# Kernel tuning notes

Measured on AMD Instinct MI355X. Metric: run time of the kernel, lower is better.

Reference implementation:

```python
import jax, jax.numpy as jnp
import numpy as np
from jax import lax

K, D = 7, 2                      # kernel_size, dilation
PAD = (K - 1) * D                # = 12, matches init padding
B, CIN, COUT, L = 8, 128, 256, 4096


def _na_indices(L2, k, d):
    """NATTEN-style dilated 1D neighborhood: key positions + rel-pos-bias indices."""
    i = jnp.arange(L2)
    r, ii = i % d, i // d
    Lg = (L2 - r + d - 1) // d                       # dilation-group lengths
    start = jnp.clip(ii - k // 2, 0, Lg - k)         # clamped window start (in-group)
    t = jnp.arange(k)
    pos = r[:, None] + d * (start[:, None] + t[None, :])        # [L2,k] key positions
    bidx = start[:, None] + t[None, :] - ii[:, None] + (k - 1)  # [L2,k] rpb index in [0,2k-2]
    return pos, bidx


def setup_inputs() -> dict:
    key = jax.random.key(0)
    ks = jax.random.split(key, 11)
    s = 0.05
    return {
        "x": jax.random.normal(ks[0], (B, CIN, L), jnp.float32),
        "conv1_v": jax.random.normal(ks[1], (COUT, CIN, K), jnp.float32) * s,
        "conv1_g": jax.random.uniform(ks[2], (COUT,), jnp.float32, 0.5, 1.5),
        "conv1_b": jax.random.normal(ks[3], (COUT,), jnp.float32) * s,
        "qkv_w": jax.random.normal(ks[4], (3 * COUT, COUT), jnp.float32) * s,
        "qkv_b": jax.random.normal(ks[5], (3 * COUT,), jnp.float32) * s,
        "rpb": jax.random.normal(ks[6], (1, 2 * K - 1), jnp.float32) * s,
        "proj_w": jax.random.normal(ks[7], (COUT, COUT), jnp.float32) * s,
        "proj_b": jax.random.normal(ks[8], (COUT,), jnp.float32) * s,
        "ds_w": jax.random.normal(ks[9], (COUT, CIN, 1), jnp.float32) * s,
        "ds_b": jax.random.normal(ks[10], (COUT,), jnp.float32) * s,
    }


def reference(x, conv1_v, conv1_g, conv1_b, qkv_w, qkv_b, rpb, proj_w, proj_b, ds_w, ds_b):
    # weight_norm: w = g * v / ||v|| over (in_ch, kernel) per out channel
    vn = jnp.sqrt(jnp.sum(conv1_v * conv1_v, axis=(1, 2), keepdims=True))
    w1 = conv1_g[:, None, None] * conv1_v / vn
    out = lax.conv_general_dilated(x, w1, (1,), [(PAD, PAD)], rhs_dilation=(D,),
                                   dimension_numbers=("NCH", "OIH", "NCH"))
    out = out + conv1_b[None, :, None]
    out = jax.nn.relu(out[:, :, :-PAD])              # chomp1 + relu (dropout = eval identity)

    # left-pad then neighborhood attention on [B, L2, C]
    h = jnp.pad(out, ((0, 0), (0, 0), (PAD, 0))).transpose(0, 2, 1)
    L2 = h.shape[1]
    qkv = h @ qkv_w.T + qkv_b
    q, k_, v = jnp.split(qkv, 3, axis=-1)            # single head, head_dim = COUT
    pos, bidx = _na_indices(L2, K, D)
    kg = k_[:, pos, :]                               # [B, L2, K, C]
    vg = v[:, pos, :]
    scores = jnp.einsum("blc,blkc->blk", q * (COUT ** -0.5), kg) + rpb[0][bidx][None]
    attn = jax.nn.softmax(scores, axis=-1)
    o = jnp.einsum("blk,blkc->blc", attn, vg) @ proj_w.T + proj_b

    out = jax.nn.relu(o.transpose(0, 2, 1)[:, :, :-PAD])   # chomp2 + relu
    res = jnp.einsum("bcl,oc->bol", x, ds_w[:, :, 0]) + ds_b[None, :, None]
    return jax.nn.relu(out + res)
```

## Files before the change

kernel.cpp:

```cpp
#include <hip/hip_runtime.h>
#include <math.h>

#define KW 7
#define PADW 12
#define BATCH 8
#define CIN 128
#define COUT 256
#define LEN 4096
#define L2V 4108
#define NQKV 768
#define KCONV 896
#define PTILE 128

typedef unsigned short u16;
typedef short v8s __attribute__((ext_vector_type(8)));
typedef float v4f __attribute__((ext_vector_type(4)));

#define KEY3(r) ((((r) & 3) ^ (((r) >> 2) & 1)))

__device__ __forceinline__ u16 f2bf(float f) {
  unsigned int x = __float_as_uint(f);
  x += 0x7fffu + ((x >> 16) & 1u);
  return (u16)(x >> 16);
}
__device__ __forceinline__ float bf2f(u16 u) {
  return __uint_as_float(((unsigned int)u) << 16);
}

__device__ __forceinline__ void gll16(const void* g, void* l) {
  __builtin_amdgcn_global_load_lds(
      (const __attribute__((address_space(1))) void*)g,
      (__attribute__((address_space(3))) void*)l, 16, 0, 0);
}

__device__ __forceinline__ void wait_vm(int n) {
  switch (n) {
    case 0:  asm volatile("s_waitcnt vmcnt(0)" ::: "memory"); break;
    case 2:  asm volatile("s_waitcnt vmcnt(2)" ::: "memory"); break;
    case 3:  asm volatile("s_waitcnt vmcnt(3)" ::: "memory"); break;
    case 10: asm volatile("s_waitcnt vmcnt(10)" ::: "memory"); break;
  }
}
#define LGKM0()  asm volatile("s_waitcnt lgkmcnt(0)" ::: "memory")
#define BARRIER() { __builtin_amdgcn_s_barrier(); asm volatile("" ::: "memory"); }

#define MFMA16(ACC, AA, BB)                                                    \
  { _Pragma("unroll") for (int fi_ = 0; fi_ < 4; ++fi_)                        \
    _Pragma("unroll") for (int fj_ = 0; fj_ < 4; ++fj_)                        \
      ACC[fi_][fj_] = __builtin_amdgcn_mfma_f32_16x16x32_bf16(                 \
          AA[fi_], BB[fj_], ACC[fi_][fj_], 0, 0, 0); }

__global__ __launch_bounds__(256) void prep_wn(
    const float* __restrict__ v, const float* __restrict__ g,
    u16* __restrict__ wt)
{
  const int c = blockIdx.x;
  const float* vo = v + (size_t)c * (CIN * KW);
  float s = 0.f;
  for (int i = threadIdx.x; i < CIN * KW; i += 256) { float t = vo[i]; s += t * t; }
#pragma unroll
  for (int off = 1; off < 64; off <<= 1) s += __shfl_xor(s, off);
  __shared__ float red[4];
  if ((threadIdx.x & 63) == 0) red[threadIdx.x >> 6] = s;
  __syncthreads();
  const float tot = red[0] + red[1] + red[2] + red[3];
  const float scale = g[c] / sqrtf(tot);
  for (int i = threadIdx.x; i < CIN * KW; i += 256) {
    const int ci = i / 7, t = i - ci * 7;
    wt[((size_t)c * KW + t) * CIN + ci] = f2bf(vo[i] * scale);
  }
}

__global__ __launch_bounds__(256) void prep_cast(
    const float* __restrict__ qw, const float* __restrict__ pw,
    const float* __restrict__ dw, u16* __restrict__ qwb,
    u16* __restrict__ pwb, u16* __restrict__ dwb)
{
  const int i4 = (blockIdx.x * 256 + threadIdx.x) * 4;
  const float* src; u16* dst; int off;
  if (i4 < 196608)      { src = qw; dst = qwb; off = i4; }
  else if (i4 < 262144) { src = pw; dst = pwb; off = i4 - 196608; }
  else                  { src = dw; dst = dwb; off = i4 - 262144; }
  const float4 vv = *(const float4*)(src + off);
  *(ushort4*)(dst + off) = make_ushort4(f2bf(vv.x), f2bf(vv.y), f2bf(vv.z), f2bf(vv.w));
}

__global__ __launch_bounds__(256) void zero_fill(
    u16* __restrict__ xT, u16* __restrict__ qkv, const float* __restrict__ qb)
{
  const int idx = blockIdx.x * 256 + threadIdx.x;
  if (idx < BATCH * PADW * CIN) {
    const int b = idx / (PADW * CIN), r = idx - b * (PADW * CIN);
    xT[(size_t)b * L2V * CIN + r] = 0;
  } else {
    const int k = idx - BATCH * PADW * CIN;
    const int b = k / (PADW * NQKV), r2 = k - b * (PADW * NQKV);
    const int row = r2 / NQKV, n = r2 - row * NQKV;
    qkv[((size_t)b * L2V + row) * NQKV + n] = f2bf(qb[n]);
  }
}

__global__ __launch_bounds__(256) void xpose(const float* __restrict__ x, u16* __restrict__ xT)
{
  const int b = blockIdx.y, p0 = blockIdx.x * 64;
  const int tx = threadIdx.x & 15, ty = threadIdx.x >> 4;
  const int p = p0 + ty * 4;
  const float* xb = x + (size_t)b * CIN * LEN;
  u16* xTb = xT + (size_t)b * L2V * CIN + (size_t)(PADW + p) * CIN;
#pragma unroll
  for (int half = 0; half < 2; ++half) {
    const int ci0 = half * 64 + tx * 4;
    float r[4][4];
#pragma unroll
    for (int i = 0; i < 4; ++i)
      *(float4*)r[i] = *(const float4*)(xb + (size_t)(ci0 + i) * LEN + p);
#pragma unroll
    for (int j = 0; j < 4; ++j)
      *(ushort4*)(xTb + (size_t)j * CIN + ci0) =
          make_ushort4(f2bf(r[0][j]), f2bf(r[1][j]), f2bf(r[2][j]), f2bf(r[3][j]));
  }
}

__global__ __launch_bounds__(512, 2) void conv_qkv_fused(
    const u16* __restrict__ wt, const u16* __restrict__ xT,
    const float* __restrict__ c1b, const u16* __restrict__ qwb,
    const float* __restrict__ qb, u16* __restrict__ qkv)
{
  const int b = blockIdx.y;
  const int p0 = blockIdx.x * PTILE;
  const int tid = threadIdx.x;
  const int w = tid >> 6, lane = tid & 63;
  const int l15 = lane & 15, kg = lane >> 4;
  const int wA = w >> 1, wB = w & 1;

  __shared__ u16 hA[PTILE * 256];
  __shared__ u16 pool[40960];

  const u16* xTb = xT + (size_t)b * L2V * CIN + (size_t)p0 * CIN;

  v4f acc[4][4];
#pragma unroll
  for (int i = 0; i < 4; ++i)
#pragma unroll
    for (int j = 0; j < 4; ++j) acc[i][j] = (v4f){0.f, 0.f, 0.f, 0.f};

  auto stageA = [&](int s, int buf) {
    const int t = s >> 2, ci0 = (s & 3) << 5;
    u16* dst = pool + buf * 12288;
#pragma unroll
    for (int i = 0; i < 2; ++i) {
      const int cidx = i * 512 + tid;
      const int row = cidx >> 2, ch = cidx & 3;
      gll16(wt + (size_t)row * KCONV + t * CIN + ci0 + ((ch ^ KEY3(row)) << 3),
            (void*)(dst + cidx * 8));
    }
    {
      const int row = tid >> 2, ch = tid & 3;
      gll16(xTb + (size_t)(2 * t + row) * CIN + ci0 + ((ch ^ KEY3(row)) << 3),
            (void*)(dst + 8192 + tid * 8));
    }
  };

  stageA(0, 0);
  stageA(1, 1);

#pragma unroll
  for (int s = 0; s < 28; ++s) {
    if (s < 27) wait_vm(3); else wait_vm(0);
    BARRIER()
    if (s < 26) stageA(s + 2, (s + 2) % 3);
    const u16* wbuf = pool + (s % 3) * 12288;
    const u16* xbuf = wbuf + 8192;
    v8s a[4], bb[4];
#pragma unroll
    for (int f = 0; f < 4; ++f) {
      const int c = wA * 64 + f * 16 + l15;
      a[f] = *(const v8s*)&wbuf[c * 32 + ((kg ^ KEY3(c)) << 3)];
      const int p = wB * 64 + f * 16 + l15;
      bb[f] = *(const v8s*)&xbuf[p * 32 + ((kg ^ KEY3(p)) << 3)];
    }
    MFMA16(acc, a, bb)
  }

#pragma unroll
  for (int fi = 0; fi < 4; ++fi) {
    const int cb = wA * 64 + fi * 16 + kg * 4;
    const float4 bv = *(const float4*)(c1b + cb);
    const int ch32 = cb >> 3, off = cb & 7;
#pragma unroll
    for (int fj = 0; fj < 4; ++fj) {
      const int p = wB * 64 + fj * 16 + l15;
      *(ushort4*)&hA[p * 256 + ((ch32 ^ (p & 7)) << 3) + off] = make_ushort4(
          f2bf(fmaxf(acc[fi][fj][0] + bv.x, 0.f)),
          f2bf(fmaxf(acc[fi][fj][1] + bv.y, 0.f)),
          f2bf(fmaxf(acc[fi][fj][2] + bv.z, 0.f)),
          f2bf(fmaxf(acc[fi][fj][3] + bv.w, 0.f)));
      acc[fi][fj] = (v4f){0.f, 0.f, 0.f, 0.f};
    }
  }
  LGKM0();
  BARRIER()

  auto stageB = [&](int it2, int buf) {
    const int nt = it2 >> 3, k0 = (it2 & 7) << 5;
    u16* dst = pool + buf * 8192;
#pragma unroll
    for (int i = 0; i < 2; ++i) {
      const int cidx = i * 512 + tid;
      const int row = cidx >> 2, ch = cidx & 3;
      gll16(qwb + (size_t)(nt * 256 + row) * COUT + k0 + ((ch ^ KEY3(row)) << 3),
            (void*)(dst + cidx * 8));
    }
  };
  stageB(0, 0);
  stageB(1, 1);

  const size_t mg0 = (size_t)b * L2V + PADW + p0;
  u16* T = pool + 24576;

#pragma unroll
  for (int it = 0; it < 24; ++it) {
    const int s = it & 7, st = it >> 3;
    if (it == 23) wait_vm(0);
    else if (it >= 8 && s <= 1) wait_vm(10);
    else wait_vm(2);
    BARRIER()
    if (it < 22) stageB(it + 2, (it + 2) % 3);
    const u16* nbuf = pool + (it % 3) * 8192;
    v8s a[4], bb[4];
#pragma unroll
    for (int f = 0; f < 4; ++f) {
      const int n = wA * 64 + f * 16 + l15;
      a[f] = *(const v8s*)&nbuf[n * 32 + ((kg ^ KEY3(n)) << 3)];
      const int m = wB * 64 + f * 16 + l15;
      bb[f] = *(const v8s*)&hA[m * 256 + ((((s << 2) + kg) ^ (m & 7)) << 3)];
    }
    MFMA16(acc, a, bb)

    if (s == 7) {
#pragma unroll
      for (int h2 = 0; h2 < 2; ++h2) {
        if ((wA >> 1) == h2) {
#pragma unroll
          for (int fi = 0; fi < 4; ++fi) {
            const int j = (wA & 1) * 64 + fi * 16 + kg * 4;
            const float4 bv = *(const float4*)(qb + st * 256 + h2 * 128 + j);
            const int jc = j >> 3, joff = j & 7;
#pragma unroll
            for (int fj = 0; fj < 4; ++fj) {
              const int m = wB * 64 + fj * 16 + l15;
              *(ushort4*)&T[m * 128 + ((jc ^ (m & 15)) << 3) + joff] = make_ushort4(
                  f2bf(acc[fi][fj][0] + bv.x), f2bf(acc[fi][fj][1] + bv.y),
                  f2bf(acc[fi][fj][2] + bv.z), f2bf(acc[fi][fj][3] + bv.w));
            }
          }
        }
        LGKM0();
        BARRIER()
#pragma unroll
        for (int i2 = 0; i2 < 4; ++i2) {
          const int chunk = i2 * 512 + tid;
          const int m = chunk >> 4, j16 = chunk & 15;
          const int4 vv = *(const int4*)&T[m * 128 + ((j16 ^ (m & 15)) << 3)];
          *(int4*)(qkv + (mg0 + m) * NQKV + st * 256 + h2 * 128 + j16 * 8) = vv;
        }
        LGKM0();
        BARRIER()
      }
#pragma unroll
      for (int fi = 0; fi < 4; ++fi)
#pragma unroll
        for (int fj = 0; fj < 4; ++fj) acc[fi][fj] = (v4f){0.f, 0.f, 0.f, 0.f};
    }
  }
}

__global__ __launch_bounds__(256) void attn_bf16(
    const u16* __restrict__ qkv, const float* __restrict__ rpb,
    u16* __restrict__ ao)
{
  const int wid = (blockIdx.x << 2) + (threadIdx.x >> 6);
  const int lane = threadIdx.x & 63;
  const int b = wid >> 12;
  const int j = wid & 4095;
  const int r = j & 1, ii = j >> 1;
  int start = ii - 3;
  start = start < 0 ? 0 : start;
  start = start > 2047 ? 2047 : start;

  const u16* base = qkv + (size_t)b * L2V * NQKV;
  const ushort4 qv = *(const ushort4*)(base + (size_t)j * NQKV + 4 * lane);
  const float q0 = bf2f(qv.x) * 0.0625f, q1 = bf2f(qv.y) * 0.0625f;
  const float q2 = bf2f(qv.z) * 0.0625f, q3 = bf2f(qv.w) * 0.0625f;

  float sc[7];
  float mx = -1e30f;
#pragma unroll
  for (int t = 0; t < 7; ++t) {
    const int pos = r + 2 * (start + t);
    const ushort4 kv = *(const ushort4*)(base + (size_t)pos * NQKV + COUT + 4 * lane);
    float s = q0 * bf2f(kv.x) + q1 * bf2f(kv.y) + q2 * bf2f(kv.z) + q3 * bf2f(kv.w);
#pragma unroll
    for (int o = 1; o < 64; o <<= 1) s += __shfl_xor(s, o);
    s += rpb[start + t - ii + 6];
    sc[t] = s;
    mx = fmaxf(mx, s);
  }
  float sum = 0.f;
#pragma unroll
  for (int t = 0; t < 7; ++t) { sc[t] = __expf(sc[t] - mx); sum += sc[t]; }
  const float inv = 1.f / sum;

  float a0 = 0.f, a1 = 0.f, a2 = 0.f, a3 = 0.f;
#pragma unroll
  for (int t = 0; t < 7; ++t) {
    const int pos = r + 2 * (start + t);
    const ushort4 vv = *(const ushort4*)(base + (size_t)pos * NQKV + 2 * COUT + 4 * lane);
    const float wgt = sc[t] * inv;
    a0 += wgt * bf2f(vv.x); a1 += wgt * bf2f(vv.y);
    a2 += wgt * bf2f(vv.z); a3 += wgt * bf2f(vv.w);
  }
  *(ushort4*)(ao + ((size_t)(b * LEN + j)) * COUT + 4 * lane) =
      make_ushort4(f2bf(a0), f2bf(a1), f2bf(a2), f2bf(a3));
}

__global__ __launch_bounds__(256, 2) void projds_gll(
    const u16* __restrict__ ao, const u16* __restrict__ pwb,
    const float* __restrict__ pb, const u16* __restrict__ xT,
    const u16* __restrict__ dwb, const float* __restrict__ db,
    float* __restrict__ out)
{
  const int b = blockIdx.z;
  const int l0 = blockIdx.x * 128, o0 = blockIdx.y * 128;
  const int tid = threadIdx.x;
  const int w = tid >> 6, lane = tid & 63;
  const int l15 = lane & 15, kg = lane >> 4;
  const int wr = w >> 1, wc = w & 1;

  __shared__ u16 sX[2][128 * 32];
  __shared__ u16 sW[2][128 * 32];

  const int arow = tid >> 2, ach = tid & 3;
  const int akey = KEY3(arow);
  const u16* aob = ao + (size_t)b * LEN * COUT;
  const u16* xTb = xT + ((size_t)b * L2V + PADW) * CIN;

  auto stage1 = [&](int s, int buf) {
#pragma unroll
    for (int i = 0; i < 2; ++i) {
      const int row = i * 64 + arow;
      const int sl = (ach ^ akey) << 3;
      gll16(aob + (size_t)(l0 + row) * COUT + (s << 5) + sl,
            (void*)&sX[buf][(i * 256 + tid) * 8]);
      gll16(pwb + (size_t)(o0 + row) * COUT + (s << 5) + sl,
            (void*)&sW[buf][(i * 256 + tid) * 8]);
    }
  };
  auto stage2 = [&](int s, int buf) {
#pragma unroll
    for (int i = 0; i < 2; ++i) {
      const int row = i * 64 + arow;
      const int sl = (ach ^ akey) << 3;
      gll16(xTb + (size_t)(l0 + row) * CIN + (s << 5) + sl,
            (void*)&sX[buf][(i * 256 + tid) * 8]);
      gll16(dwb + (size_t)(o0 + row) * CIN + (s << 5) + sl,
            (void*)&sW[buf][(i * 256 + tid) * 8]);
    }
  };

  v4f acc[4][4];
#pragma unroll
  for (int i = 0; i < 4; ++i)
#pragma unroll
    for (int j = 0; j < 4; ++j) acc[i][j] = (v4f){0.f, 0.f, 0.f, 0.f};

  stage1(0, 0);
  __syncthreads();
  for (int ss = 0; ss < 12; ++ss) {
    const int buf = ss & 1;
    if (ss < 7) stage1(ss + 1, buf ^ 1);
    else if (ss < 11) stage2(ss - 7, buf ^ 1);
    v8s a[4], bb[4];
#pragma unroll
    for (int f = 0; f < 4; ++f) {
      const int lr = wr * 64 + f * 16 + l15;
      a[f] = *(const v8s*)&sX[buf][lr * 32 + ((kg ^ KEY3(lr)) << 3)];
      const int orr = wc * 64 + f * 16 + l15;
      bb[f] = *(const v8s*)&sW[buf][orr * 32 + ((kg ^ KEY3(orr)) << 3)];
    }
#pragma unroll
    for (int fi_ = 0; fi_ < 4; ++fi_)
#pragma unroll
      for (int fj_ = 0; fj_ < 4; ++fj_)
        acc[fi_][fj_] = __builtin_amdgcn_mfma_f32_16x16x32_bf16(
            a[fi_], bb[fj_], acc[fi_][fj_], 0, 0, 0);
    if (ss == 7) {
#pragma unroll
      for (int fj = 0; fj < 4; ++fj) {
        const float pbv = pb[o0 + wc * 64 + fj * 16 + l15];
#pragma unroll
        for (int fi = 0; fi < 4; ++fi)
#pragma unroll
          for (int jj = 0; jj < 4; ++jj)
            acc[fi][fj][jj] = fmaxf(acc[fi][fj][jj] + pbv, 0.f);
      }
    }
    __syncthreads();
  }

#pragma unroll
  for (int fj = 0; fj < 4; ++fj) {
    const int o = o0 + wc * 64 + fj * 16 + l15;
    const float dbv = db[o];
    float* orow = out + ((size_t)(b * COUT + o)) * LEN;
#pragma unroll
    for (int fi = 0; fi < 4; ++fi) {
      const int lb = l0 + wr * 64 + fi * 16 + kg * 4;
      float v0 = acc[fi][fj][0] + dbv; v0 = v0 > 0.f ? v0 : 0.f;
      float v1 = acc[fi][fj][1] + dbv; v1 = v1 > 0.f ? v1 : 0.f;
      float v2 = acc[fi][fj][2] + dbv; v2 = v2 > 0.f ? v2 : 0.f;
      float v3 = acc[fi][fj][3] + dbv; v3 = v3 > 0.f ? v3 : 0.f;
      *(float4*)(orow + lb) = make_float4(v0, v1, v2, v3);
    }
  }
}

extern "C" void kernel_launch(void* const* d_in, const int* in_sizes, int n_in,
                              void* d_out, int out_size, void* d_ws, size_t ws_size,
                              hipStream_t stream)
{
  (void)in_sizes; (void)n_in; (void)out_size; (void)ws_size;
  const float* x   = (const float*)d_in[0];
  const float* c1v = (const float*)d_in[1];
  const float* c1g = (const float*)d_in[2];
  const float* c1b = (const float*)d_in[3];
  const float* qw  = (const float*)d_in[4];
  const float* qb  = (const float*)d_in[5];
  const float* rpb = (const float*)d_in[6];
  const float* pw  = (const float*)d_in[7];
  const float* pb  = (const float*)d_in[8];
  const float* dw  = (const float*)d_in[9];
  const float* db  = (const float*)d_in[10];
  float* out = (float*)d_out;

  char* ws = (char*)d_ws;
  u16* wt  = (u16*)(ws);
  u16* qwb = (u16*)(ws + 458752);
  u16* pwb = (u16*)(ws + 851968);
  u16* dwb = (u16*)(ws + 983040);
  u16* xT  = (u16*)(ws + 1048576);
  u16* qkv = (u16*)(ws + 26288128);
  u16* ao  = (u16*)(ws + 76767232);

  prep_wn<<<COUT, 256, 0, stream>>>(c1v, c1g, wt);
  prep_cast<<<288, 256, 0, stream>>>(qw, pw, dw, qwb, pwb, dwb);
  zero_fill<<<336, 256, 0, stream>>>(xT, qkv, qb);
  xpose<<<dim3(LEN / 64, BATCH), 256, 0, stream>>>(x, xT);
  conv_qkv_fused<<<dim3(LEN / PTILE, BATCH), 512, 0, stream>>>(wt, xT, c1b, qwb, qb, qkv);
  attn_bf16<<<(BATCH * LEN) / 4, 256, 0, stream>>>(qkv, rpb, ao);
  projds_gll<<<dim3(LEN / 128, COUT / 128, BATCH), 256, 0, stream>>>(ao, pwb, pb, xT, dwb, db, out);
}
```

Measured before the change: 106.1 us.

## Fold Q/K/V projections algebraically into weights to shrink the QKV GEMM

Rewrites the attention algebraically. Scores become h_j·(Wq^T Wk) h_pos plus folded bias terms, and the value and output projections are merged into a single precomputed Wp·Wv matrix applied after the attention-weighted sum of h. The fused conv kernel now emits only h and g = scaled (Wk^T Wq) h (256 columns instead of 768), and attention gathers h only once for both scores and values. This cuts GEMM work and memory traffic in the fused kernel and the attention kernel, at the cost of new prep kernels that compute the folded weights and biases, plus some bf16 rounding of the folded products.

After: 112.3 us. 5.9% more time.

```diff
diff --git a/kernel.cpp b/kernel.cpp
--- a/kernel.cpp
+++ b/kernel.cpp
@@ -8,7 +8,6 @@
 #define COUT 256
 #define LEN 4096
 #define L2V 4108
-#define NQKV 768
 #define KCONV 896
 #define PTILE 128
 
@@ -35,10 +34,9 @@
 
 __device__ __forceinline__ void wait_vm(int n) {
   switch (n) {
-    case 0:  asm volatile("s_waitcnt vmcnt(0)" ::: "memory"); break;
-    case 2:  asm volatile("s_waitcnt vmcnt(2)" ::: "memory"); break;
-    case 3:  asm volatile("s_waitcnt vmcnt(3)" ::: "memory"); break;
-    case 10: asm volatile("s_waitcnt vmcnt(10)" ::: "memory"); break;
+    case 0: asm volatile("s_waitcnt vmcnt(0)" ::: "memory"); break;
+    case 2: asm volatile("s_waitcnt vmcnt(2)" ::: "memory"); break;
+    case 3: asm volatile("s_waitcnt vmcnt(3)" ::: "memory"); break;
   }
 }
 #define LGKM0()  asm volatile("s_waitcnt lgkmcnt(0)" ::: "memory")
@@ -71,32 +69,120 @@
   }
 }
 
-__global__ __launch_bounds__(256) void prep_cast(
+__global__ __launch_bounds__(256) void prep_fold(
     const float* __restrict__ qw, const float* __restrict__ pw,
-    const float* __restrict__ dw, u16* __restrict__ qwb,
-    u16* __restrict__ pwb, u16* __restrict__ dwb)
-{
-  const int i4 = (blockIdx.x * 256 + threadIdx.x) * 4;
-  const float* src; u16* dst; int off;
-  if (i4 < 196608)      { src = qw; dst = qwb; off = i4; }
-  else if (i4 < 262144) { src = pw; dst = pwb; off = i4 - 196608; }
-  else                  { src = dw; dst = dwb; off = i4 - 262144; }
-  const float4 vv = *(const float4*)(src + off);
-  *(ushort4*)(dst + off) = make_ushort4(f2bf(vv.x), f2bf(vv.y), f2bf(vv.z), f2bf(vv.w));
-}
-
-__global__ __launch_bounds__(256) void zero_fill(
-    u16* __restrict__ xT, u16* __restrict__ qkv, const float* __restrict__ qb)
+    u16* __restrict__ gwb, u16* __restrict__ mpv)
+{
+  const int z = blockIdx.z;
+  const int d0 = blockIdx.y * 64, c0 = blockIdx.x * 64;
+  const int tid = threadIdx.x;
+  const int tx = tid & 15, ty = tid >> 4;
+  __shared__ float As[16][68], Bs[16][68];
+  float acc[4][4] = {};
+  const int idx = tid * 4;
+  const int kk4 = idx >> 6, cc4 = idx & 63;
+  const int lm = idx >> 4, lk = idx & 15;
+
+  for (int k0 = 0; k0 < 256; k0 += 16) {
+    if (z == 0) {
+      *(float4*)&As[kk4][cc4] = *(const float4*)(qw + (size_t)(256 + k0 + kk4) * 256 + d0 + cc4);
+      *(float4*)&Bs[kk4][cc4] = *(const float4*)(qw + (size_t)(k0 + kk4) * 256 + c0 + cc4);
+    } else {
+      const float4 va = *(const float4*)(pw + (size_t)(d0 + lm) * 256 + k0 + lk);
+      As[lk + 0][lm] = va.x; As[lk + 1][lm] = va.y; As[lk + 2][lm] = va.z; As[lk + 3][lm] = va.w;
+      *(float4*)&Bs[kk4][cc4] = *(const float4*)(qw + (size_t)(512 + k0 + kk4) * 256 + c0 + cc4);
+    }
+    __syncthreads();
+#pragma unroll
+    for (int kk = 0; kk < 16; ++kk) {
+      const float4 a = *(const float4*)&As[kk][ty * 4];
+      const float4 bb = *(const float4*)&Bs[kk][tx * 4];
+      const float av[4] = {a.x, a.y, a.z, a.w}, bv[4] = {bb.x, bb.y, bb.z, bb.w};
+#pragma unroll
+      for (int i = 0; i < 4; ++i)
+#pragma unroll
+        for (int j = 0; j < 4; ++j) acc[i][j] += av[i] * bv[j];
+    }
+    __syncthreads();
+  }
+  u16* dst = z ? mpv : gwb;
+  const float scale = z ? 1.f : 0.0625f;
+#pragma unroll
+  for (int i = 0; i < 4; ++i) {
+    const int d = d0 + ty * 4 + i;
+#pragma unroll
+    for (int j = 0; j < 4; ++j)
+      dst[(size_t)d * 256 + c0 + tx * 4 + j] = f2bf(acc[i][j] * scale);
+  }
+}
+
+__global__ __launch_bounds__(256) void fold_misc(
+    const float* __restrict__ qw, const float* __restrict__ qb,
+    const float* __restrict__ pw, const float* __restrict__ pb,
+    const float* __restrict__ dw, float* __restrict__ params,
+    u16* __restrict__ dwb)
+{
+  const int bid = blockIdx.x, tid = threadIdx.x;
+  if (bid >= 258) {
+    const int i = (bid - 258) * 256 + tid;
+    dwb[i] = f2bf(dw[i]);
+    return;
+  }
+  if (bid >= 2) {
+    const int o = bid - 2;
+    float part = pw[(size_t)o * 256 + tid] * qb[512 + tid];
+#pragma unroll
+    for (int off = 1; off < 64; off <<= 1) part += __shfl_xor(part, off);
+    __shared__ float red[4];
+    if ((tid & 63) == 0) red[tid >> 6] = part;
+    __syncthreads();
+    if (tid == 0) params[512 + o] = red[0] + red[1] + red[2] + red[3] + pb[o];
+    return;
+  }
+  if (bid == 1) {
+    float s0 = 0, s1 = 0, s2 = 0, s3 = 0;
+    for (int a = 0; a < 256; a += 4) {
+      s0 += qw[(size_t)(a + 0) * 256 + tid] * qb[256 + a + 0];
+      s1 += qw[(size_t)(a + 1) * 256 + tid] * qb[256 + a + 1];
+      s2 += qw[(size_t)(a + 2) * 256 + tid] * qb[256 + a + 2];
+      s3 += qw[(size_t)(a + 3) * 256 + tid] * qb[256 + a + 3];
+    }
+    params[256 + tid] = 0.0625f * (s0 + s1 + s2 + s3);
+    return;
+  }
+  float s0 = 0, s1 = 0, s2 = 0, s3 = 0;
+  for (int a = 0; a < 256; a += 4) {
+    s0 += qw[(size_t)(256 + a + 0) * 256 + tid] * qb[a + 0];
+    s1 += qw[(size_t)(256 + a + 1) * 256 + tid] * qb[a + 1];
+    s2 += qw[(size_t)(256 + a + 2) * 256 + tid] * qb[a + 2];
+    s3 += qw[(size_t)(256 + a + 3) * 256 + tid] * qb[a + 3];
+  }
+  params[tid] = 0.0625f * (s0 + s1 + s2 + s3);
+  float part = qb[tid] * qb[256 + tid];
+#pragma unroll
+  for (int off = 1; off < 64; off <<= 1) part += __shfl_xor(part, off);
+  __shared__ float red2[4];
+  if ((tid & 63) == 0) red2[tid >> 6] = part;
+  __syncthreads();
+  if (tid == 0) params[768] = 0.0625f * (red2[0] + red2[1] + red2[2] + red2[3]);
+}
+
+__global__ __launch_bounds__(256) void zero_fill2(
+    u16* __restrict__ xT, u16* __restrict__ h, u16* __restrict__ g,
+    const float* __restrict__ params)
 {
   const int idx = blockIdx.x * 256 + threadIdx.x;
-  if (idx < BATCH * PADW * CIN) {
-    const int b = idx / (PADW * CIN), r = idx - b * (PADW * CIN);
+  if (idx < 12288) {
+    const int b = idx / 1536, r = idx - b * 1536;
     xT[(size_t)b * L2V * CIN + r] = 0;
+  } else if (idx < 36864) {
+    const int k = idx - 12288;
+    const int b = k / 3072, r = k - b * 3072;
+    h[(size_t)b * L2V * COUT + r] = 0;
   } else {
-    const int k = idx - BATCH * PADW * CIN;
-    const int b = k / (PADW * NQKV), r2 = k - b * (PADW * NQKV);
-    const int row = r2 / NQKV, n = r2 - row * NQKV;
-    qkv[((size_t)b * L2V + row) * NQKV + n] = f2bf(qb[n]);
+    const int k = idx - 36864;
+    const int b = k / 3072, r = k - b * 3072;
+    g[(size_t)b * L2V * COUT + r] = f2bf(params[r & 255]);
   }
 }
 
@@ -121,10 +207,11 @@
   }
 }
 
-__global__ __launch_bounds__(512, 2) void conv_qkv_fused(
+__global__ __launch_bounds__(512, 2) void conv_g_fused(
     const u16* __restrict__ wt, const u16* __restrict__ xT,
-    const float* __restrict__ c1b, const u16* __restrict__ qwb,
-    const float* __restrict__ qb, u16* __restrict__ qkv)
+    const float* __restrict__ c1b, const u16* __restrict__ gwb,
+    const float* __restrict__ params, u16* __restrict__ hout,
+    u16* __restrict__ gout)
 {
   const int b = blockIdx.y;
   const int p0 = blockIdx.x * PTILE;
@@ -201,32 +288,34 @@
   LGKM0();
   BARRIER()
 
-  auto stageB = [&](int it2, int buf) {
-    const int nt = it2 >> 3, k0 = (it2 & 7) << 5;
+  const size_t mg0h = (size_t)b * L2V + PADW + p0;
+#pragma unroll
+  for (int i = 0; i < 8; ++i) {
+    const int chunk = i * 512 + tid;
+    const int p = chunk >> 5, ci = chunk & 31;
+    const int4 vv = *(const int4*)&hA[p * 256 + ((ci ^ (p & 7)) << 3)];
+    *(int4*)(hout + (mg0h + p) * COUT + ci * 8) = vv;
+  }
+
+  auto stageB = [&](int s, int buf) {
     u16* dst = pool + buf * 8192;
 #pragma unroll
     for (int i = 0; i < 2; ++i) {
       const int cidx = i * 512 + tid;
       const int row = cidx >> 2, ch = cidx & 3;
-      gll16(qwb + (size_t)(nt * 256 + row) * COUT + k0 + ((ch ^ KEY3(row)) << 3),
+      gll16(gwb + (size_t)row * COUT + (s << 5) + ((ch ^ KEY3(row)) << 3),
             (void*)(dst + cidx * 8));
     }
   };
   stageB(0, 0);
   stageB(1, 1);
 
-  const size_t mg0 = (size_t)b * L2V + PADW + p0;
-  u16* T = pool + 24576;
-
-#pragma unroll
-  for (int it = 0; it < 24; ++it) {
-    const int s = it & 7, st = it >> 3;
-    if (it == 23) wait_vm(0);
-    else if (it >= 8 && s <= 1) wait_vm(10);
-    else wait_vm(2);
+#pragma unroll
+  for (int s = 0; s < 8; ++s) {
+    if (s < 7) wait_vm(2); else wait_vm(0);
     BARRIER()
-    if (it < 22) stageB(it + 2, (it + 2) % 3);
-    const u16* nbuf = pool + (it % 3) * 8192;
+    if (s < 6) stageB(s + 2, (s + 2) % 3);
+    const u16* nbuf = pool + (s % 3) * 8192;
     v8s a[4], bb[4];
 #pragma unroll
     for (int f = 0; f < 4; ++f) {
@@ -236,48 +325,44 @@
       bb[f] = *(const v8s*)&hA[m * 256 + ((((s << 2) + kg) ^ (m & 7)) << 3)];
     }
     MFMA16(acc, a, bb)
-
-    if (s == 7) {
-#pragma unroll
-      for (int h2 = 0; h2 < 2; ++h2) {
-        if ((wA >> 1) == h2) {
-#pragma unroll
-          for (int fi = 0; fi < 4; ++fi) {
-            const int j = (wA & 1) * 64 + fi * 16 + kg * 4;
-            const float4 bv = *(const float4*)(qb + st * 256 + h2 * 128 + j);
-            const int jc = j >> 3, joff = j & 7;
-#pragma unroll
-            for (int fj = 0; fj < 4; ++fj) {
-              const int m = wB * 64 + fj * 16 + l15;
-              *(ushort4*)&T[m * 128 + ((jc ^ (m & 15)) << 3) + joff] = make_ushort4(
-                  f2bf(acc[fi][fj][0] + bv.x), f2bf(acc[fi][fj][1] + bv.y),
-                  f2bf(acc[fi][fj][2] + bv.z), f2bf(acc[fi][fj][3] + bv.w));
-            }
-          }
+  }
+
+  u16* T = pool + 24576;
+#pragma unroll
+  for (int h2 = 0; h2 < 2; ++h2) {
+    if ((wA >> 1) == h2) {
+#pragma unroll
+      for (int fi = 0; fi < 4; ++fi) {
+        const int jj = (wA & 1) * 64 + fi * 16 + kg * 4;
+        const float4 bv = *(const float4*)(params + h2 * 128 + jj);
+        const int jc = jj >> 3, joff = jj & 7;
+#pragma unroll
+        for (int fj = 0; fj < 4; ++fj) {
+          const int m = wB * 64 + fj * 16 + l15;
+          *(ushort4*)&T[m * 128 + ((jc ^ (m & 15)) << 3) + joff] = make_ushort4(
+              f2bf(acc[fi][fj][0] + bv.x), f2bf(acc[fi][fj][1] + bv.y),
+              f2bf(acc[fi][fj][2] + bv.z), f2bf(acc[fi][fj][3] + bv.w));
         }
-        LGKM0();
-        BARRIER()
-#pragma unroll
-        for (int i2 = 0; i2 < 4; ++i2) {
-          const int chunk = i2 * 512 + tid;
-          const int m = chunk >> 4, j16 = chunk & 15;
-          const int4 vv = *(const int4*)&T[m * 128 + ((j16 ^ (m & 15)) << 3)];
-          *(int4*)(qkv + (mg0 + m) * NQKV + st * 256 + h2 * 128 + j16 * 8) = vv;
-        }
-        LGKM0();
-        BARRIER()
       }
-#pragma unroll
-      for (int fi = 0; fi < 4; ++fi)
-#pragma unroll
-        for (int fj = 0; fj < 4; ++fj) acc[fi][fj] = (v4f){0.f, 0.f, 0.f, 0.f};
-    }
-  }
-}
-
-__global__ __launch_bounds__(256) void attn_bf16(
-    const u16* __restrict__ qkv, const float* __restrict__ rpb,
-    u16* __restrict__ ao)
+    }
+    LGKM0();
+    BARRIER()
+#pragma unroll
+    for (int i2 = 0; i2 < 4; ++i2) {
+      const int chunk = i2 * 512 + tid;
+      const int m = chunk >> 4, j16 = chunk & 15;
+      const int4 vv = *(const int4*)&T[m * 128 + ((j16 ^ (m & 15)) << 3)];
+      *(int4*)(gout + (mg0h + m) * COUT + h2 * 128 + j16 * 8) = vv;
+    }
+    LGKM0();
+    BARRIER()
+  }
+}
+
+__global__ __launch_bounds__(256) void attn_v2(
+    const u16* __restrict__ h, const u16* __restrict__ g,
+    const float* __restrict__ params, const float* __restrict__ rpb,
+    u16* __restrict__ sout)
 {
   const int wid = (blockIdx.x << 2) + (threadIdx.x >> 6);
   const int lane = threadIdx.x & 63;
@@ -288,21 +373,32 @@
   start = start < 0 ? 0 : start;
   start = start > 2047 ? 2047 : start;
 
-  const u16* base = qkv + (size_t)b * L2V * NQKV;
-  const ushort4 qv = *(const ushort4*)(base + (size_t)j * NQKV + 4 * lane);
-  const float q0 = bf2f(qv.x) * 0.0625f, q1 = bf2f(qv.y) * 0.0625f;
-  const float q2 = bf2f(qv.z) * 0.0625f, q3 = bf2f(qv.w) * 0.0625f;
-
+  const u16* hb = h + (size_t)b * L2V * COUT;
+  const u16* gb = g + (size_t)b * L2V * COUT;
+
+  const ushort4 gv = *(const ushort4*)(gb + (size_t)j * COUT + 4 * lane);
+  const float g0 = bf2f(gv.x), g1 = bf2f(gv.y), g2 = bf2f(gv.z), g3 = bf2f(gv.w);
+  const ushort4 hj = *(const ushort4*)(hb + (size_t)j * COUT + 4 * lane);
+  const float4 wv = *(const float4*)(params + 256 + 4 * lane);
+  float e = bf2f(hj.x) * wv.x + bf2f(hj.y) * wv.y +
+            bf2f(hj.z) * wv.z + bf2f(hj.w) * wv.w;
+#pragma unroll
+  for (int o = 1; o < 64; o <<= 1) e += __shfl_xor(e, o);
+  e += params[768];
+
+  float hp[7][4];
   float sc[7];
   float mx = -1e30f;
 #pragma unroll
   for (int t = 0; t < 7; ++t) {
     const int pos = r + 2 * (start + t);
-    const ushort4 kv = *(const ushort4*)(base + (size_t)pos * NQKV + COUT + 4 * lane);
-    float s = q0 * bf2f(kv.x) + q1 * bf2f(kv.y) + q2 * bf2f(kv.z) + q3 * bf2f(kv.w);
+    const ushort4 hv = *(const ushort4*)(hb + (size_t)pos * COUT + 4 * lane);
+    hp[t][0] = bf2f(hv.x); hp[t][1] = bf2f(hv.y);
+    hp[t][2] = bf2f(hv.z); hp[t][3] = bf2f(hv.w);
+    float s = g0 * hp[t][0] + g1 * hp[t][1] + g2 * hp[t][2] + g3 * hp[t][3];
 #pragma unroll
     for (int o = 1; o < 64; o <<= 1) s += __shfl_xor(s, o);
-    s += rpb[start + t - ii + 6];
+    s += e + rpb[start + t - ii + 6];
     sc[t] = s;
     mx = fmaxf(mx, s);
   }
@@ -314,13 +410,11 @@
   float a0 = 0.f, a1 = 0.f, a2 = 0.f, a3 = 0.f;
 #pragma unroll
   for (int t = 0; t < 7; ++t) {
-    const int pos = r + 2 * (start + t);
-    const ushort4 vv = *(const ushort4*)(base + (size_t)pos * NQKV + 2 * COUT + 4 * lane);
     const float wgt = sc[t] * inv;
-    a0 += wgt * bf2f(vv.x); a1 += wgt * bf2f(vv.y);
-    a2 += wgt * bf2f(vv.z); a3 += wgt * bf2f(vv.w);
-  }
-  *(ushort4*)(ao + ((size_t)(b * LEN + j)) * COUT + 4 * lane) =
+    a0 += wgt * hp[t][0]; a1 += wgt * hp[t][1];
+    a2 += wgt * hp[t][2]; a3 += wgt * hp[t][3];
+  }
+  *(ushort4*)(sout + ((size_t)(b * LEN + j)) * COUT + 4 * lane) =
       make_ushort4(f2bf(a0), f2bf(a1), f2bf(a2), f2bf(a3));
 }
 
@@ -444,19 +538,23 @@
   float* out = (float*)d_out;
 
   char* ws = (char*)d_ws;
-  u16* wt  = (u16*)(ws);
-  u16* qwb = (u16*)(ws + 458752);
-  u16* pwb = (u16*)(ws + 851968);
-  u16* dwb = (u16*)(ws + 983040);
-  u16* xT  = (u16*)(ws + 1048576);
-  u16* qkv = (u16*)(ws + 26288128);
-  u16* ao  = (u16*)(ws + 76767232);
+  u16*   wt     = (u16*)(ws);
+  u16*   gwb    = (u16*)(ws + 458752);
+  u16*   mpv    = (u16*)(ws + 589824);
+  u16*   dwb    = (u16*)(ws + 720896);
+  float* params = (float*)(ws + 786432);
+  u16*   xT     = (u16*)(ws + 1048576);
+  u16*   h      = (u16*)(ws + 9461760);
+  u16*   g      = (u16*)(ws + 26288128);
+  u16*   s      = (u16*)(ws + 43114496);
 
   prep_wn<<<COUT, 256, 0, stream>>>(c1v, c1g, wt);
-  prep_cast<<<288, 256, 0, stream>>>(qw, pw, dw, qwb, pwb, dwb);
-  zero_fill<<<336, 256, 0, stream>>>(xT, qkv, qb);
+  prep_fold<<<dim3(4, 4, 2), 256, 0, stream>>>(qw, pw, gwb, mpv);
+  fold_misc<<<386, 256, 0, stream>>>(qw, qb, pw, pb, dw, params, dwb);
+  zero_fill2<<<240, 256, 0, stream>>>(xT, h, g, params);
   xpose<<<dim3(LEN / 64, BATCH), 256, 0, stream>>>(x, xT);
-  conv_qkv_fused<<<dim3(LEN / PTILE, BATCH), 512, 0, stream>>>(wt, xT, c1b, qwb, qb, qkv);
-  attn_bf16<<<(BATCH * LEN) / 4, 256, 0, stream>>>(qkv, rpb, ao);
-  projds_gll<<<dim3(LEN / 128, COUT / 128, BATCH), 256, 0, stream>>>(ao, pwb, pb, xT, dwb, db, out);
-}
+  conv_g_fused<<<dim3(LEN / PTILE, BATCH), 512, 0, stream>>>(wt, xT, c1b, gwb, params, h, g);
+  attn_v2<<<(BATCH * LEN) / 4, 256, 0, stream>>>(h, g, params, rpb, s);
+  projds_gll<<<dim3(LEN / 128, COUT / 128, BATCH), 256, 0, stream>>>(
+      s, mpv, params + 512, xT, dwb, db, out);
+}
```
